# Performance work log

Hardware: AMD Instinct MI355X
Metric: run time of the kernel (lower is better)

The kernel has to match this reference:

```python
import jax, jax.numpy as jnp
import numpy as np

H = 8   # n_heads
C = 2   # top-k scale factor: topk = int(C * log(L))


def setup_inputs() -> dict:
    key = jax.random.key(0)
    k1, k2, k3 = jax.random.split(key, 3)
    B, L, D = 16, 512, 4096  # L == D // H required by the original broadcasting
    Q = jax.random.normal(k1, (B, L, D), dtype=jnp.float32)
    K = jax.random.normal(k2, (B, L, D), dtype=jnp.float32)
    V = jax.random.normal(k3, (B, L, D), dtype=jnp.float32)
    return {"Q": Q, "K": K, "V": V}


def _autocorrelation(Q, K, V):
    B, L, D = Q.shape
    d = D // H
    # [B,L,D] -> [B,H,L,d]
    q = Q.reshape(B, L, H, d).transpose(0, 2, 1, 3)
    k = K.reshape(B, L, H, d).transpose(0, 2, 1, 3)
    v = V.reshape(B, L, H, d).transpose(0, 2, 1, 3)
    # FFT-based autocorrelation along the time axis (per head, per channel)
    qf = jnp.fft.fft(q, axis=2)
    kf = jnp.fft.fft(k, axis=2)
    corr = jnp.fft.ifft(qf * jnp.conj(kf), axis=2).real  # [B,H,L,d]
    topk = int(C * np.log(L))  # static: 12 for L=512
    # top-k delays per (batch, head, channel): move L to last axis
    w, idx = jax.lax.top_k(corr.transpose(0, 1, 3, 2), topk)  # [B,H,d,topk]
    w = jax.nn.softmax(w, axis=-1)
    pos = jnp.arange(L)[:, None]  # [L,1]
    out = jnp.zeros_like(v)       # [B,H,L,d]
    # small fixed loop over topk ~ O(log L) delays: gather + scale + accumulate
    for i in range(topk):
        g = jnp.minimum(idx[:, :, None, :, i] + pos, L - 1)        # [B,H,L,d]
        out = out + w[:, :, None, :, i] * jnp.take_along_axis(v, g, axis=2)
    return out.transpose(0, 2, 1, 3).reshape(B, L, D)


def reference(Q, K, V):
    return _autocorrelation(Q, K, V)
```

## Files before the change

### kernel.cpp

```cpp
#include <hip/hip_runtime.h>
#include <stdint.h>

#define L_LEN 512
#define D_DIM 4096
#define H_NUM 8
#define B_NUM 16
#define TOPK  12

typedef float f32x4 __attribute__((ext_vector_type(4)));


#define QA(G) (qbase + (((((uint32_t)(G)) & 127u) + ((((uint32_t)(G)) & 127u) >> 3)) << 4))

#define MAC4x8(QA_, QB_, QC_, KK_) do {                                       \
    acc0 = fmaf(QA_.x, KK_.x, acc0); acc0 = fmaf(QA_.y, KK_.y, acc0);         \
    acc0 = fmaf(QA_.z, KK_.z, acc0); acc0 = fmaf(QA_.w, KK_.w, acc0);         \
    acc1 = fmaf(QA_.y, KK_.x, acc1); acc1 = fmaf(QA_.z, KK_.y, acc1);         \
    acc1 = fmaf(QA_.w, KK_.z, acc1); acc1 = fmaf(QB_.x, KK_.w, acc1);         \
    acc2 = fmaf(QA_.z, KK_.x, acc2); acc2 = fmaf(QA_.w, KK_.y, acc2);         \
    acc2 = fmaf(QB_.x, KK_.z, acc2); acc2 = fmaf(QB_.y, KK_.w, acc2);         \
    acc3 = fmaf(QA_.w, KK_.x, acc3); acc3 = fmaf(QB_.x, KK_.y, acc3);         \
    acc3 = fmaf(QB_.y, KK_.z, acc3); acc3 = fmaf(QB_.z, KK_.w, acc3);         \
    acc4 = fmaf(QB_.x, KK_.x, acc4); acc4 = fmaf(QB_.y, KK_.y, acc4);         \
    acc4 = fmaf(QB_.z, KK_.z, acc4); acc4 = fmaf(QB_.w, KK_.w, acc4);         \
    acc5 = fmaf(QB_.y, KK_.x, acc5); acc5 = fmaf(QB_.z, KK_.y, acc5);         \
    acc5 = fmaf(QB_.w, KK_.z, acc5); acc5 = fmaf(QC_.x, KK_.w, acc5);         \
    acc6 = fmaf(QB_.z, KK_.x, acc6); acc6 = fmaf(QB_.w, KK_.y, acc6);         \
    acc6 = fmaf(QC_.x, KK_.z, acc6); acc6 = fmaf(QC_.y, KK_.w, acc6);         \
    acc7 = fmaf(QB_.w, KK_.x, acc7); acc7 = fmaf(QC_.x, KK_.y, acc7);         \
    acc7 = fmaf(QC_.y, KK_.z, acc7); acc7 = fmaf(QC_.z, KK_.w, acc7);         \
  } while (0)

#define ITER3(A0,A1,A2,A3, B0,B1,B2,B3, C0,C1,C2,C3) do {                    \
    const uint32_t a0_ = QA(gnext);                                          \
    const uint32_t a1_ = QA(gnext + 1);                                      \
    const uint32_t a2_ = QA(gnext + 2);                                      \
    const uint32_t a3_ = QA(gnext + 3);                                      \
    asm volatile(                                                            \
      "ds_read_b128 %0, %8\n\t"                                              \
      "ds_read_b128 %1, %9\n\t"                                              \
      "ds_read_b128 %2, %10\n\t"                                             \
      "ds_read_b128 %3, %11\n\t"                                             \
      "ds_read_b128 %4, %12\n\t"                                             \
      "ds_read_b128 %5, %12 offset:16\n\t"                                   \
      "ds_read_b128 %6, %12 offset:32\n\t"                                   \
      "ds_read_b128 %7, %12 offset:48\n\t"                                   \
      "s_waitcnt lgkmcnt(0)"                                                 \
      : "=&v"(C0), "=&v"(C1), "=&v"(C2), "=&v"(C3),                          \
        "=&v"(k0), "=&v"(k1), "=&v"(k2), "=&v"(k3)                           \
      : "v"(a0_), "v"(a1_), "v"(a2_), "v"(a3_), "v"(kcur)                    \
      : "memory");                                                           \
    MAC4x8(A0, A1, A2, k0);                                                  \
    MAC4x8(A1, A2, A3, k1);                                                  \
    MAC4x8(A2, A3, B0, k2);                                                  \
    MAC4x8(A3, B0, B1, k3);                                                  \
    gnext += 4; kcur += 64;                                                  \
  } while (0)

__global__ __launch_bounds__(512, 4) void corr_topk_kernel(
    const float* __restrict__ Q, const float* __restrict__ K,
    float* __restrict__ ws_w, int* __restrict__ ws_i)
{
  __shared__ __align__(16) float qs[8][576];
  __shared__ __align__(16) float ks[8][512];

  const int tid = threadIdx.x;
  const int bid = blockIdx.x;
  const int work = (bid & 7) * 1024 + (bid >> 3);
  const int bh   = work >> 6;
  const int c0   = (work & 63) * 8;

  const size_t base = (size_t)(bh >> 3) * (size_t)(L_LEN * D_DIM)
                    + (size_t)(bh & 7) * 512 + c0;

  #pragma unroll
  for (int rep = 0; rep < 2; ++rep) {
    const int idx  = rep * 512 + tid;
    const int t    = idx >> 1;
    const int half = idx & 1;
    const float4 qv = *(const float4*)(Q + base + (size_t)t * D_DIM + half * 4);
    const float4 kv = *(const float4*)(K + base + (size_t)t * D_DIM + half * 4);
    const int g  = t >> 2;
    const int pw = ((g + (g >> 3)) << 2) | (t & 3);
    const int cb = half * 4;
    const float qa[4] = {qv.x, qv.y, qv.z, qv.w};
    const float ka[4] = {kv.x, kv.y, kv.z, kv.w};
    #pragma unroll
    for (int j = 0; j < 4; ++j) {
      qs[cb + j][pw] = qa[j];
      ks[cb + j][t]  = ka[j];
    }
  }
  __syncthreads();

  const int wv   = __builtin_amdgcn_readfirstlane(tid >> 6);
  const int lane = tid & 63;
  const int tau0 = lane * 8;
  const int gq   = lane * 2;

  const uint32_t qbase = (uint32_t)(uintptr_t)(&qs[wv][0]);
  const uint32_t kbase = (uint32_t)(uintptr_t)(&ks[wv][0]);

  float acc0 = 0.f, acc1 = 0.f, acc2 = 0.f, acc3 = 0.f;
  float acc4 = 0.f, acc5 = 0.f, acc6 = 0.f, acc7 = 0.f;
  f32x4 wA0, wA1, wA2, wA3, wB0, wB1, wB2, wB3, wC0, wC1, wC2, wC3;
  f32x4 k0, k1, k2, k3;

  {
    const uint32_t p0 = QA(gq),     p1 = QA(gq + 1);
    const uint32_t p2 = QA(gq + 2), p3 = QA(gq + 3);
    const uint32_t p4 = QA(gq + 4), p5 = QA(gq + 5);
    const uint32_t p6 = QA(gq + 6), p7 = QA(gq + 7);
    asm volatile(
      "ds_read_b128 %0, %8\n\t"
      "ds_read_b128 %1, %9\n\t"
      "ds_read_b128 %2, %10\n\t"
      "ds_read_b128 %3, %11\n\t"
      "ds_read_b128 %4, %12\n\t"
      "ds_read_b128 %5, %13\n\t"
      "ds_read_b128 %6, %14\n\t"
      "ds_read_b128 %7, %15\n\t"
      "s_waitcnt lgkmcnt(0)"
      : "=&v"(wA0), "=&v"(wA1), "=&v"(wA2), "=&v"(wA3),
        "=&v"(wB0), "=&v"(wB1), "=&v"(wB2), "=&v"(wB3)
      : "v"(p0), "v"(p1), "v"(p2), "v"(p3), "v"(p4), "v"(p5), "v"(p6), "v"(p7)
      : "memory");
  }

  uint32_t gnext = (uint32_t)(gq + 8);
  uint32_t kcur  = kbase;

  #pragma unroll 1
  for (int i = 0; i < 30; i += 3) {
    ITER3(wA0,wA1,wA2,wA3, wB0,wB1,wB2,wB3, wC0,wC1,wC2,wC3);
    ITER3(wB0,wB1,wB2,wB3, wC0,wC1,wC2,wC3, wA0,wA1,wA2,wA3);
    ITER3(wC0,wC1,wC2,wC3, wA0,wA1,wA2,wA3, wB0,wB1,wB2,wB3);
  }
  ITER3(wA0,wA1,wA2,wA3, wB0,wB1,wB2,wB3, wC0,wC1,wC2,wC3);
  ITER3(wB0,wB1,wB2,wB3, wC0,wC1,wC2,wC3, wA0,wA1,wA2,wA3);

  float acc[8] = {acc0, acc1, acc2, acc3, acc4, acc5, acc6, acc7};

  float bv[TOPK]; int bi[TOPK];
  #pragma unroll
  for (int s = 0; s < TOPK; ++s) {
    float lv = acc[0]; int li = 0;
    #pragma unroll
    for (int i = 1; i < 8; ++i) if (acc[i] > lv) { lv = acc[i]; li = i; }
    int gi = tau0 + li;
    #pragma unroll
    for (int off = 32; off >= 1; off >>= 1) {
      const float ov = __shfl_xor(lv, off, 64);
      const int   oi = __shfl_xor(gi, off, 64);
      if (ov > lv || (ov == lv && oi < gi)) { lv = ov; gi = oi; }
    }
    bv[s] = lv; bi[s] = gi;
    const int slot = gi - tau0;
    #pragma unroll
    for (int i = 0; i < 8; ++i) acc[i] = (slot == i) ? -3.4e38f : acc[i];
  }

  float e[TOPK]; float sum = 0.f;
  #pragma unroll
  for (int s = 0; s < TOPK; ++s) { e[s] = expf(bv[s] - bv[0]); sum += e[s]; }
  const float inv = 1.f / sum;

  if (lane == 0) {
    const int g = (bh * 512 + c0 + wv) * TOPK;
    #pragma unroll
    for (int s = 0; s < TOPK; ++s) { ws_w[g + s] = e[s] * inv; ws_i[g + s] = bi[s]; }
  }
}

__global__ __launch_bounds__(512, 4) void gather_kernel(
    const float* __restrict__ V, const float* __restrict__ ws_w,
    const int* __restrict__ ws_i, float* __restrict__ out)
{
  __shared__ __align__(16) float vs[512][32];

  const int tid = threadIdx.x;
  const int bid = blockIdx.x;
  const int work = (bid & 7) * 256 + (bid >> 3);
  const int b  = work >> 7;
  const int dg = work & 127;
  const int d0 = dg * 32;
  const int h  = d0 >> 9;
  const int c0 = d0 & 511;

  const size_t vcol = (size_t)b * (size_t)(L_LEN * D_DIM) + d0;

  const int cl   = tid & 31;
  const int tsub = tid >> 5;

  float4 stga, stgb;
  const int e0 = tid, e1 = 512 + tid;
  const int ra0 = e0 >> 3, qa0 = (e0 & 7) * 4;
  const int rb0 = e1 >> 3, qb0 = (e1 & 7) * 4;

  stga = *(const float4*)(V + vcol + (size_t)(384 + ra0) * D_DIM + qa0);
  stgb = *(const float4*)(V + vcol + (size_t)(384 + rb0) * D_DIM + qb0);

  const int g = ((b * 8 + h) * 512 + c0 + cl) * TOPK;
  float w[TOPK]; int r0[TOPK];
  #pragma unroll
  for (int s = 0; s < TOPK; ++s) { w[s] = ws_w[g + s]; r0[s] = ws_i[g + s]; }

  const size_t ob = vcol + cl;

  #pragma unroll 1
  for (int ph = 3; ph >= 0; --ph) {
    *(float4*)(&vs[ph * 128 + ra0][qa0]) = stga;
    *(float4*)(&vs[ph * 128 + rb0][qb0]) = stgb;
    if (ph > 0) {
      stga = *(const float4*)(V + vcol + (size_t)((ph - 1) * 128 + ra0) * D_DIM + qa0);
      stgb = *(const float4*)(V + vcol + (size_t)((ph - 1) * 128 + rb0) * D_DIM + qb0);
    }
    asm volatile("s_waitcnt lgkmcnt(0)" ::: "memory");
    __builtin_amdgcn_s_barrier();
    asm volatile("" ::: "memory");

    #pragma unroll
    for (int k8 = 0; k8 < 8; ++k8) {
      const int t = ph * 128 + (k8 << 4) + tsub;
      float a = 0.f;
      #pragma unroll
      for (int s = 0; s < TOPK; ++s) {
        int r = r0[s] + t;
        r = r > (L_LEN - 1) ? (L_LEN - 1) : r;
        a = fmaf(w[s], vs[r][cl], a);
      }
      out[ob + (size_t)t * D_DIM] = a;
    }
  }
}

extern "C" void kernel_launch(void* const* d_in, const int* in_sizes, int n_in,
                              void* d_out, int out_size, void* d_ws, size_t ws_size,
                              hipStream_t stream)
{
  const float* Q = (const float*)d_in[0];
  const float* K = (const float*)d_in[1];
  const float* V = (const float*)d_in[2];
  float* out = (float*)d_out;

  float* ws_w = (float*)d_ws;
  int*   ws_i = (int*)((char*)d_ws + (size_t)B_NUM * H_NUM * 512 * TOPK * sizeof(float));

  corr_topk_kernel<<<dim3(B_NUM * H_NUM * 64), dim3(512), 0, stream>>>(Q, K, ws_w, ws_i);
  gather_kernel<<<dim3(B_NUM * H_NUM * 16), dim3(512), 0, stream>>>(V, ws_w, ws_i, out);
}
```

Baseline: 836.8 us.

## Compute sixteen lags per lane with half-wave per channel in correlation kernel

```diff
diff --git a/kernel.cpp b/kernel.cpp
--- a/kernel.cpp
+++ b/kernel.cpp
@@ -12,26 +12,42 @@
 
 #define QA(G) (qbase + (((((uint32_t)(G)) & 127u) + ((((uint32_t)(G)) & 127u) >> 3)) << 4))
 
-#define MAC4x8(QA_, QB_, QC_, KK_) do {                                       \
-    acc0 = fmaf(QA_.x, KK_.x, acc0); acc0 = fmaf(QA_.y, KK_.y, acc0);         \
-    acc0 = fmaf(QA_.z, KK_.z, acc0); acc0 = fmaf(QA_.w, KK_.w, acc0);         \
-    acc1 = fmaf(QA_.y, KK_.x, acc1); acc1 = fmaf(QA_.z, KK_.y, acc1);         \
-    acc1 = fmaf(QA_.w, KK_.z, acc1); acc1 = fmaf(QB_.x, KK_.w, acc1);         \
-    acc2 = fmaf(QA_.z, KK_.x, acc2); acc2 = fmaf(QA_.w, KK_.y, acc2);         \
-    acc2 = fmaf(QB_.x, KK_.z, acc2); acc2 = fmaf(QB_.y, KK_.w, acc2);         \
-    acc3 = fmaf(QA_.w, KK_.x, acc3); acc3 = fmaf(QB_.x, KK_.y, acc3);         \
-    acc3 = fmaf(QB_.y, KK_.z, acc3); acc3 = fmaf(QB_.z, KK_.w, acc3);         \
-    acc4 = fmaf(QB_.x, KK_.x, acc4); acc4 = fmaf(QB_.y, KK_.y, acc4);         \
-    acc4 = fmaf(QB_.z, KK_.z, acc4); acc4 = fmaf(QB_.w, KK_.w, acc4);         \
-    acc5 = fmaf(QB_.y, KK_.x, acc5); acc5 = fmaf(QB_.z, KK_.y, acc5);         \
-    acc5 = fmaf(QB_.w, KK_.z, acc5); acc5 = fmaf(QC_.x, KK_.w, acc5);         \
-    acc6 = fmaf(QB_.z, KK_.x, acc6); acc6 = fmaf(QB_.w, KK_.y, acc6);         \
-    acc6 = fmaf(QC_.x, KK_.z, acc6); acc6 = fmaf(QC_.y, KK_.w, acc6);         \
-    acc7 = fmaf(QB_.w, KK_.x, acc7); acc7 = fmaf(QC_.x, KK_.y, acc7);         \
-    acc7 = fmaf(QC_.y, KK_.z, acc7); acc7 = fmaf(QC_.z, KK_.w, acc7);         \
+#define MAC4x16(QA_, QB_, QC_, QD_, QE_, KK_) do {                            \
+    acc0  = fmaf(QA_.x, KK_.x, acc0);  acc0  = fmaf(QA_.y, KK_.y, acc0);      \
+    acc0  = fmaf(QA_.z, KK_.z, acc0);  acc0  = fmaf(QA_.w, KK_.w, acc0);      \
+    acc1  = fmaf(QA_.y, KK_.x, acc1);  acc1  = fmaf(QA_.z, KK_.y, acc1);      \
+    acc1  = fmaf(QA_.w, KK_.z, acc1);  acc1  = fmaf(QB_.x, KK_.w, acc1);      \
+    acc2  = fmaf(QA_.z, KK_.x, acc2);  acc2  = fmaf(QA_.w, KK_.y, acc2);      \
+    acc2  = fmaf(QB_.x, KK_.z, acc2);  acc2  = fmaf(QB_.y, KK_.w, acc2);      \
+    acc3  = fmaf(QA_.w, KK_.x, acc3);  acc3  = fmaf(QB_.x, KK_.y, acc3);      \
+    acc3  = fmaf(QB_.y, KK_.z, acc3);  acc3  = fmaf(QB_.z, KK_.w, acc3);      \
+    acc4  = fmaf(QB_.x, KK_.x, acc4);  acc4  = fmaf(QB_.y, KK_.y, acc4);      \
+    acc4  = fmaf(QB_.z, KK_.z, acc4);  acc4  = fmaf(QB_.w, KK_.w, acc4);      \
+    acc5  = fmaf(QB_.y, KK_.x, acc5);  acc5  = fmaf(QB_.z, KK_.y, acc5);      \
+    acc5  = fmaf(QB_.w, KK_.z, acc5);  acc5  = fmaf(QC_.x, KK_.w, acc5);      \
+    acc6  = fmaf(QB_.z, KK_.x, acc6);  acc6  = fmaf(QB_.w, KK_.y, acc6);      \
+    acc6  = fmaf(QC_.x, KK_.z, acc6);  acc6  = fmaf(QC_.y, KK_.w, acc6);      \
+    acc7  = fmaf(QB_.w, KK_.x, acc7);  acc7  = fmaf(QC_.x, KK_.y, acc7);      \
+    acc7  = fmaf(QC_.y, KK_.z, acc7);  acc7  = fmaf(QC_.z, KK_.w, acc7);      \
+    acc8  = fmaf(QC_.x, KK_.x, acc8);  acc8  = fmaf(QC_.y, KK_.y, acc8);      \
+    acc8  = fmaf(QC_.z, KK_.z, acc8);  acc8  = fmaf(QC_.w, KK_.w, acc8);      \
+    acc9  = fmaf(QC_.y, KK_.x, acc9);  acc9  = fmaf(QC_.z, KK_.y, acc9);      \
+    acc9  = fmaf(QC_.w, KK_.z, acc9);  acc9  = fmaf(QD_.x, KK_.w, acc9);      \
+    acc10 = fmaf(QC_.z, KK_.x, acc10); acc10 = fmaf(QC_.w, KK_.y, acc10);     \
+    acc10 = fmaf(QD_.x, KK_.z, acc10); acc10 = fmaf(QD_.y, KK_.w, acc10);     \
+    acc11 = fmaf(QC_.w, KK_.x, acc11); acc11 = fmaf(QD_.x, KK_.y, acc11);     \
+    acc11 = fmaf(QD_.y, KK_.z, acc11); acc11 = fmaf(QD_.z, KK_.w, acc11);     \
+    acc12 = fmaf(QD_.x, KK_.x, acc12); acc12 = fmaf(QD_.y, KK_.y, acc12);     \
+    acc12 = fmaf(QD_.z, KK_.z, acc12); acc12 = fmaf(QD_.w, KK_.w, acc12);     \
+    acc13 = fmaf(QD_.y, KK_.x, acc13); acc13 = fmaf(QD_.z, KK_.y, acc13);     \
+    acc13 = fmaf(QD_.w, KK_.z, acc13); acc13 = fmaf(QE_.x, KK_.w, acc13);     \
+    acc14 = fmaf(QD_.z, KK_.x, acc14); acc14 = fmaf(QD_.w, KK_.y, acc14);     \
+    acc14 = fmaf(QE_.x, KK_.z, acc14); acc14 = fmaf(QE_.y, KK_.w, acc14);     \
+    acc15 = fmaf(QD_.w, KK_.x, acc15); acc15 = fmaf(QE_.x, KK_.y, acc15);     \
+    acc15 = fmaf(QE_.y, KK_.z, acc15); acc15 = fmaf(QE_.z, KK_.w, acc15);     \
   } while (0)
 
-#define ITER3(A0,A1,A2,A3, B0,B1,B2,B3, C0,C1,C2,C3) do {                    \
+#define ITERX(A0,A1,A2,A3, B0,B1,B2,B3, C0,C1,C2,C3) do {                    \
     const uint32_t a0_ = QA(gnext);                                          \
     const uint32_t a1_ = QA(gnext + 1);                                      \
     const uint32_t a2_ = QA(gnext + 2);                                      \
@@ -48,16 +64,16 @@
       "s_waitcnt lgkmcnt(0)"                                                 \
       : "=&v"(C0), "=&v"(C1), "=&v"(C2), "=&v"(C3),                          \
         "=&v"(k0), "=&v"(k1), "=&v"(k2), "=&v"(k3)                           \
-      : "v"(a0_), "v"(a1_), "v"(a2_), "v"(a3_), "v"(kcur)                    \
+      : "v"(a0_), "v"(a1_), "v"(a2_), "v"(a3_), "v"(kptr)                    \
       : "memory");                                                           \
-    MAC4x8(A0, A1, A2, k0);                                                  \
-    MAC4x8(A1, A2, A3, k1);                                                  \
-    MAC4x8(A2, A3, B0, k2);                                                  \
-    MAC4x8(A3, B0, B1, k3);                                                  \
-    gnext += 4; kcur += 64;                                                  \
+    MAC4x16(A0, A1, A2, A3, B0, k0);                                         \
+    MAC4x16(A1, A2, A3, B0, B1, k1);                                         \
+    MAC4x16(A2, A3, B0, B1, B2, k2);                                         \
+    MAC4x16(A3, B0, B1, B2, B3, k3);                                         \
+    gnext += 4; kptr += 64;                                                  \
   } while (0)
 
-__global__ __launch_bounds__(512, 4) void corr_topk_kernel(
+__global__ __launch_bounds__(256, 4) void corr_topk_kernel(
     const float* __restrict__ Q, const float* __restrict__ K,
     float* __restrict__ ws_w, int* __restrict__ ws_i)
 {
@@ -74,8 +90,8 @@
                     + (size_t)(bh & 7) * 512 + c0;
 
   #pragma unroll
-  for (int rep = 0; rep < 2; ++rep) {
-    const int idx  = rep * 512 + tid;
+  for (int rep = 0; rep < 4; ++rep) {
+    const int idx  = rep * 256 + tid;
     const int t    = idx >> 1;
     const int half = idx & 1;
     const float4 qv = *(const float4*)(Q + base + (size_t)t * D_DIM + half * 4);
@@ -93,16 +109,20 @@
   }
   __syncthreads();
 
-  const int wv   = __builtin_amdgcn_readfirstlane(tid >> 6);
+  const int wv   = tid >> 6;
   const int lane = tid & 63;
-  const int tau0 = lane * 8;
-  const int gq   = lane * 2;
-
-  const uint32_t qbase = (uint32_t)(uintptr_t)(&qs[wv][0]);
-  const uint32_t kbase = (uint32_t)(uintptr_t)(&ks[wv][0]);
-
-  float acc0 = 0.f, acc1 = 0.f, acc2 = 0.f, acc3 = 0.f;
-  float acc4 = 0.f, acc5 = 0.f, acc6 = 0.f, acc7 = 0.f;
+  const int m    = lane & 31;
+  const int ch   = wv * 2 + (lane >> 5);
+  const int tau0 = m * 16;
+  const int gq   = m * 4;
+
+  const uint32_t qbase = (uint32_t)(uintptr_t)(&qs[ch][0]);
+  uint32_t       kptr  = (uint32_t)(uintptr_t)(&ks[ch][0]);
+
+  float acc0  = 0.f, acc1  = 0.f, acc2  = 0.f, acc3  = 0.f;
+  float acc4  = 0.f, acc5  = 0.f, acc6  = 0.f, acc7  = 0.f;
+  float acc8  = 0.f, acc9  = 0.f, acc10 = 0.f, acc11 = 0.f;
+  float acc12 = 0.f, acc13 = 0.f, acc14 = 0.f, acc15 = 0.f;
   f32x4 wA0, wA1, wA2, wA3, wB0, wB1, wB2, wB3, wC0, wC1, wC2, wC3;
   f32x4 k0, k1, k2, k3;
 
@@ -128,36 +148,36 @@
   }
 
   uint32_t gnext = (uint32_t)(gq + 8);
-  uint32_t kcur  = kbase;
 
   #pragma unroll 1
   for (int i = 0; i < 30; i += 3) {
-    ITER3(wA0,wA1,wA2,wA3, wB0,wB1,wB2,wB3, wC0,wC1,wC2,wC3);
-    ITER3(wB0,wB1,wB2,wB3, wC0,wC1,wC2,wC3, wA0,wA1,wA2,wA3);
-    ITER3(wC0,wC1,wC2,wC3, wA0,wA1,wA2,wA3, wB0,wB1,wB2,wB3);
-  }
-  ITER3(wA0,wA1,wA2,wA3, wB0,wB1,wB2,wB3, wC0,wC1,wC2,wC3);
-  ITER3(wB0,wB1,wB2,wB3, wC0,wC1,wC2,wC3, wA0,wA1,wA2,wA3);
-
-  float acc[8] = {acc0, acc1, acc2, acc3, acc4, acc5, acc6, acc7};
+    ITERX(wA0,wA1,wA2,wA3, wB0,wB1,wB2,wB3, wC0,wC1,wC2,wC3);
+    ITERX(wB0,wB1,wB2,wB3, wC0,wC1,wC2,wC3, wA0,wA1,wA2,wA3);
+    ITERX(wC0,wC1,wC2,wC3, wA0,wA1,wA2,wA3, wB0,wB1,wB2,wB3);
+  }
+  ITERX(wA0,wA1,wA2,wA3, wB0,wB1,wB2,wB3, wC0,wC1,wC2,wC3);
+  ITERX(wB0,wB1,wB2,wB3, wC0,wC1,wC2,wC3, wA0,wA1,wA2,wA3);
+
+  float acc[16] = {acc0, acc1, acc2,  acc3,  acc4,  acc5,  acc6,  acc7,
+                   acc8, acc9, acc10, acc11, acc12, acc13, acc14, acc15};
 
   float bv[TOPK]; int bi[TOPK];
   #pragma unroll
   for (int s = 0; s < TOPK; ++s) {
     float lv = acc[0]; int li = 0;
     #pragma unroll
-    for (int i = 1; i < 8; ++i) if (acc[i] > lv) { lv = acc[i]; li = i; }
+    for (int i = 1; i < 16; ++i) if (acc[i] > lv) { lv = acc[i]; li = i; }
     int gi = tau0 + li;
     #pragma unroll
-    for (int off = 32; off >= 1; off >>= 1) {
-      const float ov = __shfl_xor(lv, off, 64);
-      const int   oi = __shfl_xor(gi, off, 64);
+    for (int off = 16; off >= 1; off >>= 1) {
+      const float ov = __shfl_xor(lv, off, 32);
+      const int   oi = __shfl_xor(gi, off, 32);
       if (ov > lv || (ov == lv && oi < gi)) { lv = ov; gi = oi; }
     }
     bv[s] = lv; bi[s] = gi;
     const int slot = gi - tau0;
     #pragma unroll
-    for (int i = 0; i < 8; ++i) acc[i] = (slot == i) ? -3.4e38f : acc[i];
+    for (int i = 0; i < 16; ++i) acc[i] = (slot == i) ? -3.4e38f : acc[i];
   }
 
   float e[TOPK]; float sum = 0.f;
@@ -165,8 +185,8 @@
   for (int s = 0; s < TOPK; ++s) { e[s] = expf(bv[s] - bv[0]); sum += e[s]; }
   const float inv = 1.f / sum;
 
-  if (lane == 0) {
-    const int g = (bh * 512 + c0 + wv) * TOPK;
+  if (m == 0) {
+    const int g = (bh * 512 + c0 + ch) * TOPK;
     #pragma unroll
     for (int s = 0; s < TOPK; ++s) { ws_w[g + s] = e[s] * inv; ws_i[g + s] = bi[s]; }
   }
@@ -246,6 +266,6 @@
   float* ws_w = (float*)d_ws;
   int*   ws_i = (int*)((char*)d_ws + (size_t)B_NUM * H_NUM * 512 * TOPK * sizeof(float));
 
-  corr_topk_kernel<<<dim3(B_NUM * H_NUM * 64), dim3(512), 0, stream>>>(Q, K, ws_w, ws_i);
+  corr_topk_kernel<<<dim3(B_NUM * H_NUM * 64), dim3(256), 0, stream>>>(Q, K, ws_w, ws_i);
   gather_kernel<<<dim3(B_NUM * H_NUM * 16), dim3(512), 0, stream>>>(V, ws_w, ws_i, out);
 }
```

Measured after the change: 765.3 us. 1.09x faster.
